# Performance work log

Measured on AMD Instinct MI355X. Metric: run time of the kernel, lower is better.

## Reference

```python
import jax, jax.numpy as jnp
import numpy as np

NL, B, L1, L2, D = 4, 64, 256, 256, 1024
LOGIT_SCALE = 1.0
BN_EPS = 1e-8


def setup_inputs() -> dict:
    key = jax.random.key(0)
    k1, k2, k3, k4, k5, k6 = jax.random.split(key, 6)
    reps1 = jax.random.normal(k1, (NL, B, L1, D), dtype=jnp.float32)
    reps2 = jax.random.normal(k2, (NL, B, L2, D), dtype=jnp.float32)
    len1 = jax.random.randint(k3, (B,), 1, L1 + 1)
    len2 = jax.random.randint(k4, (B,), 1, L2 + 1)
    w = jax.random.normal(k5, (1, NL), dtype=jnp.float32) * 0.1
    b = jax.random.normal(k6, (1,), dtype=jnp.float32) * 0.1
    return {"reps1": reps1, "reps2": reps2, "len1": len1, "len2": len2, "w": w, "b": b}


def reference(reps1, reps2, len1, len2, w, b):
    # reps: (NL, B, L, D) hidden states of selected layers, already (B-major per layer)
    neg = jnp.finfo(reps1.dtype).min
    # cosine-normalize along feature dim
    h1 = reps1 / jnp.linalg.norm(reps1, axis=-1, keepdims=True)
    h2 = reps2 / jnp.linalg.norm(reps2, axis=-1, keepdims=True)
    # similarity matrices for all layers at once: (NL, B, L1, L2)
    dots = jnp.einsum("lbid,lbjd->lbij", h1, h2)
    # ragged validity masks
    mask1 = jnp.arange(L1)[None, :] < len1[:, None]  # (B, L1)
    mask2 = jnp.arange(L2)[None, :] < len2[:, None]  # (B, L2)
    n1 = len1.astype(dots.dtype)
    n2 = len2.astype(dots.dtype)
    # max over valid rows i, mean over valid cols j  -> s1 (NL, B)
    max_i = jnp.max(jnp.where(mask1[None, :, :, None], dots, neg), axis=2)  # (NL,B,L2)
    s1 = jnp.sum(jnp.where(mask2[None], max_i, 0.0), axis=2) / n2[None]
    # max over valid cols j, mean over valid rows i  -> s2 (NL, B)
    max_j = jnp.max(jnp.where(mask2[None, :, None, :], dots, neg), axis=3)  # (NL,B,L1)
    s2 = jnp.sum(jnp.where(mask1[None], max_j, 0.0), axis=2) / n1[None]
    # harmonic mean (F1)
    feat = (2.0 * s1 * s2 / (s1 + s2)).T  # (B, NL)
    # BatchNorm1d(affine=False), training mode: batch stats, biased variance
    mean = jnp.mean(feat, axis=0, keepdims=True)
    var = jnp.mean((feat - mean) ** 2, axis=0, keepdims=True)
    feat = (feat - mean) / jnp.sqrt(var + BN_EPS)
    # final linear head + logit scale -> (B,)
    return LOGIT_SCALE * (feat @ w.T + b)[:, 0]
```

## Files before the change

kernel.cpp:

```cpp
#include <hip/hip_runtime.h>

#define NLAYERS 4
#define BATCH   64
#define LEN1    256
#define LEN2    256
#define DIM     1024
#define BKK     32
#define NKT     (DIM / BKK)
#define MHALF   128
#define PITCH   40

typedef _Float16 f16x8 __attribute__((ext_vector_type(8)));
typedef float    f32x4 __attribute__((ext_vector_type(4)));

__device__ __forceinline__ unsigned enc_f32(float v) {
  unsigned u = __float_as_uint(v);
  return (u & 0x80000000u) ? ~u : (u | 0x80000000u);
}
__device__ __forceinline__ float dec_f32(unsigned u) {
  return (u & 0x80000000u) ? __uint_as_float(u & 0x7fffffffu)
                           : __uint_as_float(~u);
}

__global__ __launch_bounds__(512, 4)
void bs_main(const float* __restrict__ reps1, const float* __restrict__ reps2,
             const int* __restrict__ len1, const int* __restrict__ len2,
             unsigned* __restrict__ colmax, float* __restrict__ s2acc) {
  __shared__ _Float16 Ah[2][MHALF * PITCH];
  __shared__ _Float16 Bh[2][LEN2 * PITCH];
  __shared__ float ssq1[MHALF];
  __shared__ float ssq2[LEN2];
  __shared__ float rowp[MHALF][4];
  __shared__ float colp[LEN2][2];
  __shared__ float redbuf[8];

  const int bid  = blockIdx.x;
  const int pair = ((bid >> 4) << 3) | (bid & 7);
  const int half = (bid >> 3) & 1;
  const int nl   = pair >> 6;
  const int bb   = pair & 63;
  const float* gA = reps1 + (size_t)pair * LEN1 * DIM + (size_t)half * MHALF * DIM;
  const float* gB = reps2 + (size_t)pair * LEN2 * DIM;

  const int tid  = threadIdx.x;
  const int lane = tid & 63;
  const int wid  = tid >> 6;
  const int wm   = wid >> 2;
  const int wn   = wid & 3;
  const int li   = lane & 15;
  const int lh   = lane >> 4;

  if (tid < MHALF) ssq1[tid] = 0.0f;
  if (tid >= 128 && tid < 384) ssq2[tid - 128] = 0.0f;

  f32x4 acc[4][4];
  #pragma unroll
  for (int a = 0; a < 4; ++a)
    #pragma unroll
    for (int c = 0; c < 4; ++c) acc[a][c] = 0.0f;

  float pssqA = 0.f, pssqB = 0.f;
  const int rA = tid >> 2;
  const int cA = (tid & 3) * 8;
  const int rB = tid >> 1;
  const int cB = (tid & 1) * 16;

  float4 ra[2], rb[4];

  auto issue_loads = [&](int kt) {
    const float4* a4 = (const float4*)(gA + (size_t)rA * DIM + kt * BKK + cA);
    ra[0] = a4[0];  ra[1] = a4[1];
    const float4* b4 = (const float4*)(gB + (size_t)rB * DIM + kt * BKK + cB);
    rb[0] = b4[0];  rb[1] = b4[1];  rb[2] = b4[2];  rb[3] = b4[3];
  };

  auto convert_write = [&](int buf) {
    {
      const float f0 = ra[0].x, f1 = ra[0].y, f2 = ra[0].z, f3 = ra[0].w;
      const float f4 = ra[1].x, f5 = ra[1].y, f6 = ra[1].z, f7 = ra[1].w;
      pssqA += f0*f0 + f1*f1 + f2*f2 + f3*f3 + f4*f4 + f5*f5 + f6*f6 + f7*f7;
      f16x8 hv;
      hv[0] = (_Float16)f0; hv[1] = (_Float16)f1; hv[2] = (_Float16)f2; hv[3] = (_Float16)f3;
      hv[4] = (_Float16)f4; hv[5] = (_Float16)f5; hv[6] = (_Float16)f6; hv[7] = (_Float16)f7;
      *(f16x8*)&Ah[buf][rA * PITCH + cA] = hv;
    }
    #pragma unroll
    for (int q = 0; q < 2; ++q) {
      const float f0 = rb[2*q].x,   f1 = rb[2*q].y,   f2 = rb[2*q].z,   f3 = rb[2*q].w;
      const float f4 = rb[2*q+1].x, f5 = rb[2*q+1].y, f6 = rb[2*q+1].z, f7 = rb[2*q+1].w;
      pssqB += f0*f0 + f1*f1 + f2*f2 + f3*f3 + f4*f4 + f5*f5 + f6*f6 + f7*f7;
      f16x8 hv;
      hv[0] = (_Float16)f0; hv[1] = (_Float16)f1; hv[2] = (_Float16)f2; hv[3] = (_Float16)f3;
      hv[4] = (_Float16)f4; hv[5] = (_Float16)f5; hv[6] = (_Float16)f6; hv[7] = (_Float16)f7;
      *(f16x8*)&Bh[buf][rB * PITCH + cB + 8*q] = hv;
    }
  };

  issue_loads(0);
  convert_write(0);
  __syncthreads();

  for (int kt = 0; kt < NKT; ++kt) {
    const int cur = kt & 1;
    const bool more = (kt + 1 < NKT);
    if (more) issue_loads(kt + 1);

    const _Float16* AhC = Ah[cur];
    const _Float16* BhC = Bh[cur];
    f16x8 af[4];
    #pragma unroll
    for (int fm = 0; fm < 4; ++fm) {
      const int r = wm * 64 + fm * 16 + li;
      af[fm] = *(const f16x8*)&AhC[r * PITCH + lh * 8];
    }
    #pragma unroll
    for (int fn = 0; fn < 4; ++fn) {
      const int r = wn * 64 + fn * 16 + li;
      const f16x8 bf = *(const f16x8*)&BhC[r * PITCH + lh * 8];
      #pragma unroll
      for (int fm = 0; fm < 4; ++fm)
        acc[fm][fn] = __builtin_amdgcn_mfma_f32_16x16x32_f16(af[fm], bf, acc[fm][fn], 0, 0, 0);
    }

    if (more) convert_write(cur ^ 1);
    __syncthreads();
  }

  atomicAdd(&ssq1[rA], pssqA);
  atomicAdd(&ssq2[rB], pssqB);
  __syncthreads();
  if (tid < MHALF) ssq1[tid] = 1.0f / sqrtf(ssq1[tid]);
  if (tid >= 128 && tid < 384) ssq2[tid - 128] = 1.0f / sqrtf(ssq2[tid - 128]);
  __syncthreads();

  const int n1 = len1[bb];
  const int n2 = len2[bb];

  float rn2v[4];
  bool  jv[4];
  #pragma unroll
  for (int fn = 0; fn < 4; ++fn) {
    const int j = wn * 64 + fn * 16 + li;
    rn2v[fn] = ssq2[j];
    jv[fn]   = (j < n2);
  }
  float rn1v[4][4];
  bool  iv[4][4];
  #pragma unroll
  for (int fm = 0; fm < 4; ++fm)
    #pragma unroll
    for (int rg = 0; rg < 4; ++rg) {
      const int i = wm * 64 + fm * 16 + lh * 4 + rg;
      rn1v[fm][rg] = ssq1[i];
      iv[fm][rg]   = (half * MHALF + i) < n1;
    }

  const float NEG = -3.402823466e38f;
  float rowm[4][4];
  float colm[4];
  #pragma unroll
  for (int fm = 0; fm < 4; ++fm)
    #pragma unroll
    for (int rg = 0; rg < 4; ++rg) rowm[fm][rg] = NEG;
  #pragma unroll
  for (int fn = 0; fn < 4; ++fn) colm[fn] = NEG;

  #pragma unroll
  for (int fm = 0; fm < 4; ++fm)
    #pragma unroll
    for (int fn = 0; fn < 4; ++fn)
      #pragma unroll
      for (int rg = 0; rg < 4; ++rg) {
        const float v = acc[fm][fn][rg] * rn1v[fm][rg] * rn2v[fn];
        if (jv[fn] && v > rowm[fm][rg]) rowm[fm][rg] = v;
        if (iv[fm][rg] && v > colm[fn]) colm[fn] = v;
      }

  #pragma unroll
  for (int m = 1; m <= 8; m <<= 1)
    #pragma unroll
    for (int fm = 0; fm < 4; ++fm)
      #pragma unroll
      for (int rg = 0; rg < 4; ++rg) {
        const float o = __shfl_xor(rowm[fm][rg], m, 64);
        rowm[fm][rg] = fmaxf(rowm[fm][rg], o);
      }
  #pragma unroll
  for (int m = 16; m <= 32; m <<= 1)
    #pragma unroll
    for (int fn = 0; fn < 4; ++fn) {
      const float o = __shfl_xor(colm[fn], m, 64);
      colm[fn] = fmaxf(colm[fn], o);
    }

  if (li == 0)
    #pragma unroll
    for (int fm = 0; fm < 4; ++fm)
      #pragma unroll
      for (int rg = 0; rg < 4; ++rg)
        rowp[wm * 64 + fm * 16 + lh * 4 + rg][wn] = rowm[fm][rg];
  if (lh == 0)
    #pragma unroll
    for (int fn = 0; fn < 4; ++fn)
      colp[wn * 64 + fn * 16 + li][wm] = colm[fn];
  __syncthreads();

  float c2 = 0.f;
  if (tid < MHALF) {
    const float rm = fmaxf(fmaxf(rowp[tid][0], rowp[tid][1]),
                           fmaxf(rowp[tid][2], rowp[tid][3]));
    if (half * MHALF + tid < n1) c2 = rm;
  }
  #pragma unroll
  for (int m = 1; m <= 32; m <<= 1) c2 += __shfl_xor(c2, m, 64);
  if (lane == 0) redbuf[wid] = c2;

  if (tid < LEN2) {
    const float cm = fmaxf(colp[tid][0], colp[tid][1]);
    atomicMax(&colmax[pair * LEN2 + tid], enc_f32(cm));
  }
  __syncthreads();
  if (tid == 0) {
    float s = 0.f;
    #pragma unroll
    for (int i = 0; i < 8; ++i) s += redbuf[i];
    atomicAdd(&s2acc[pair], s);
  }
}

__global__ void bs_combine(const unsigned* __restrict__ colmax,
                           const float* __restrict__ s2acc,
                           const int* __restrict__ len1, const int* __restrict__ len2,
                           float* __restrict__ feat) {
  __shared__ float part[4];
  const int p   = blockIdx.x;
  const int tid = threadIdx.x;
  const int bb  = p & 63;
  const int nl  = p >> 6;
  const int n1  = len1[bb];
  const int n2  = len2[bb];

  float c = 0.f;
  if (tid < n2) c = dec_f32(colmax[p * LEN2 + tid]);
  #pragma unroll
  for (int m = 1; m <= 32; m <<= 1) c += __shfl_xor(c, m, 64);
  if ((tid & 63) == 0) part[tid >> 6] = c;
  __syncthreads();
  if (tid == 0) {
    const float s1 = (part[0] + part[1] + part[2] + part[3]) / (float)n2;
    const float s2 = s2acc[p] / (float)n1;
    feat[bb * NLAYERS + nl] = 2.0f * s1 * s2 / (s1 + s2);
  }
}

__global__ void bs_head(const float* __restrict__ feat, const float* __restrict__ w,
                        const float* __restrict__ bias, float* __restrict__ out) {
  __shared__ float lds[NLAYERS][BATCH];
  const int tid = threadIdx.x;
  const int nl  = tid >> 6;
  const int b   = tid & 63;

  const float x = feat[b * NLAYERS + nl];
  float s = x;
  #pragma unroll
  for (int m = 1; m <= 32; m <<= 1) s += __shfl_xor(s, m, 64);
  const float mean = s / 64.0f;
  const float d = x - mean;
  float v = d * d;
  #pragma unroll
  for (int m = 1; m <= 32; m <<= 1) v += __shfl_xor(v, m, 64);
  const float var = v / 64.0f;
  const float y = d / sqrtf(var + 1e-8f);

  lds[nl][b] = y * w[nl];
  __syncthreads();
  if (tid < 64)
    out[tid] = lds[0][tid] + lds[1][tid] + lds[2][tid] + lds[3][tid] + bias[0];
}

extern "C" void kernel_launch(void* const* d_in, const int* in_sizes, int n_in,
                              void* d_out, int out_size, void* d_ws, size_t ws_size,
                              hipStream_t stream) {
  const float* reps1 = (const float*)d_in[0];
  const float* reps2 = (const float*)d_in[1];
  const int*   len1  = (const int*)d_in[2];
  const int*   len2  = (const int*)d_in[3];
  const float* w     = (const float*)d_in[4];
  const float* bias  = (const float*)d_in[5];

  unsigned* colmax = (unsigned*)d_ws;
  float*    s2acc  = (float*)((char*)d_ws + 256 * 256 * 4);
  float*    feat   = s2acc + 256;

  hipMemsetAsync(d_ws, 0, 256 * 256 * 4 + 2 * 256 * 4, stream);

  bs_main<<<2 * NLAYERS * BATCH, 512, 0, stream>>>(reps1, reps2, len1, len2,
                                                   colmax, s2acc);
  bs_combine<<<NLAYERS * BATCH, 256, 0, stream>>>(colmax, s2acc, len1, len2, feat);
  bs_head<<<1, 256, 0, stream>>>(feat, w, bias, (float*)d_out);
}
```

Baseline: 126.1 us.

## Process full 256x256 pair per 1024-thread block, dropping combine kernel and atomics

Each block now handles one whole (layer, batch) pair with 1024 threads (16 waves) instead of splitting rows across two 512-thread blocks. B is no longer loaded twice from global memory, so the global atomicMax on encoded column maxima, the workspace memset and the separate combine kernel all go away. Row and column reductions finish inside the block, which writes the F1 feature directly. The cost is a grid of 256 blocks on 256 CUs with larger LDS use per block, and fewer blocks to hide latency.

```diff
diff --git a/kernel.cpp b/kernel.cpp
--- a/kernel.cpp
+++ b/kernel.cpp
@@ -7,40 +7,28 @@
 #define DIM     1024
 #define BKK     32
 #define NKT     (DIM / BKK)
-#define MHALF   128
 #define PITCH   40
 
 typedef _Float16 f16x8 __attribute__((ext_vector_type(8)));
 typedef float    f32x4 __attribute__((ext_vector_type(4)));
 
-__device__ __forceinline__ unsigned enc_f32(float v) {
-  unsigned u = __float_as_uint(v);
-  return (u & 0x80000000u) ? ~u : (u | 0x80000000u);
-}
-__device__ __forceinline__ float dec_f32(unsigned u) {
-  return (u & 0x80000000u) ? __uint_as_float(u & 0x7fffffffu)
-                           : __uint_as_float(~u);
-}
-
-__global__ __launch_bounds__(512, 4)
+__global__ __launch_bounds__(1024, 4)
 void bs_main(const float* __restrict__ reps1, const float* __restrict__ reps2,
              const int* __restrict__ len1, const int* __restrict__ len2,
-             unsigned* __restrict__ colmax, float* __restrict__ s2acc) {
-  __shared__ _Float16 Ah[2][MHALF * PITCH];
+             float* __restrict__ feat) {
+  __shared__ _Float16 Ah[2][LEN1 * PITCH];
   __shared__ _Float16 Bh[2][LEN2 * PITCH];
-  __shared__ float ssq1[MHALF];
+  __shared__ float ssq1[LEN1];
   __shared__ float ssq2[LEN2];
-  __shared__ float rowp[MHALF][4];
-  __shared__ float colp[LEN2][2];
-  __shared__ float redbuf[8];
-
-  const int bid  = blockIdx.x;
-  const int pair = ((bid >> 4) << 3) | (bid & 7);
-  const int half = (bid >> 3) & 1;
-  const int nl   = pair >> 6;
-  const int bb   = pair & 63;
-  const float* gA = reps1 + (size_t)pair * LEN1 * DIM + (size_t)half * MHALF * DIM;
-  const float* gB = reps2 + (size_t)pair * LEN2 * DIM;
+  __shared__ float rowp[LEN1][4];
+  __shared__ float colp[LEN2][4];
+  __shared__ float redbuf[32];
+
+  const int bid = blockIdx.x;
+  const int nl  = bid >> 6;
+  const int bb  = bid & 63;
+  const float* gA = reps1 + (size_t)bid * LEN1 * DIM;
+  const float* gB = reps2 + (size_t)bid * LEN2 * DIM;
 
   const int tid  = threadIdx.x;
   const int lane = tid & 63;
@@ -50,8 +38,8 @@
   const int li   = lane & 15;
   const int lh   = lane >> 4;
 
-  if (tid < MHALF) ssq1[tid] = 0.0f;
-  if (tid >= 128 && tid < 384) ssq2[tid - 128] = 0.0f;
+  if (tid < 256)                  ssq1[tid] = 0.0f;
+  else if (tid < 512)             ssq2[tid - 256] = 0.0f;
 
   f32x4 acc[4][4];
   #pragma unroll
@@ -60,21 +48,20 @@
     for (int c = 0; c < 4; ++c) acc[a][c] = 0.0f;
 
   float pssqA = 0.f, pssqB = 0.f;
-  const int rA = tid >> 2;
-  const int cA = (tid & 3) * 8;
-  const int rB = tid >> 1;
-  const int cB = (tid & 1) * 16;
-
-  float4 ra[2], rb[4];
+  const int rS = tid >> 2;
+  const int cS = (tid & 3) * 8;
+
+  float4 ra[2], rb[2];
 
   auto issue_loads = [&](int kt) {
-    const float4* a4 = (const float4*)(gA + (size_t)rA * DIM + kt * BKK + cA);
+    const float4* a4 = (const float4*)(gA + (size_t)rS * DIM + kt * BKK + cS);
     ra[0] = a4[0];  ra[1] = a4[1];
-    const float4* b4 = (const float4*)(gB + (size_t)rB * DIM + kt * BKK + cB);
-    rb[0] = b4[0];  rb[1] = b4[1];  rb[2] = b4[2];  rb[3] = b4[3];
+    const float4* b4 = (const float4*)(gB + (size_t)rS * DIM + kt * BKK + cS);
+    rb[0] = b4[0];  rb[1] = b4[1];
   };
 
   auto convert_write = [&](int buf) {
+    const int idx = rS * PITCH + cS;
     {
       const float f0 = ra[0].x, f1 = ra[0].y, f2 = ra[0].z, f3 = ra[0].w;
       const float f4 = ra[1].x, f5 = ra[1].y, f6 = ra[1].z, f7 = ra[1].w;
@@ -82,17 +69,16 @@
       f16x8 hv;
       hv[0] = (_Float16)f0; hv[1] = (_Float16)f1; hv[2] = (_Float16)f2; hv[3] = (_Float16)f3;
       hv[4] = (_Float16)f4; hv[5] = (_Float16)f5; hv[6] = (_Float16)f6; hv[7] = (_Float16)f7;
-      *(f16x8*)&Ah[buf][rA * PITCH + cA] = hv;
-    }
-    #pragma unroll
-    for (int q = 0; q < 2; ++q) {
-      const float f0 = rb[2*q].x,   f1 = rb[2*q].y,   f2 = rb[2*q].z,   f3 = rb[2*q].w;
-      const float f4 = rb[2*q+1].x, f5 = rb[2*q+1].y, f6 = rb[2*q+1].z, f7 = rb[2*q+1].w;
+      *(f16x8*)&Ah[buf][idx] = hv;
+    }
+    {
+      const float f0 = rb[0].x, f1 = rb[0].y, f2 = rb[0].z, f3 = rb[0].w;
+      const float f4 = rb[1].x, f5 = rb[1].y, f6 = rb[1].z, f7 = rb[1].w;
       pssqB += f0*f0 + f1*f1 + f2*f2 + f3*f3 + f4*f4 + f5*f5 + f6*f6 + f7*f7;
       f16x8 hv;
       hv[0] = (_Float16)f0; hv[1] = (_Float16)f1; hv[2] = (_Float16)f2; hv[3] = (_Float16)f3;
       hv[4] = (_Float16)f4; hv[5] = (_Float16)f5; hv[6] = (_Float16)f6; hv[7] = (_Float16)f7;
-      *(f16x8*)&Bh[buf][rB * PITCH + cB + 8*q] = hv;
+      *(f16x8*)&Bh[buf][idx] = hv;
     }
   };
 
@@ -126,11 +112,11 @@
     __syncthreads();
   }
 
-  atomicAdd(&ssq1[rA], pssqA);
-  atomicAdd(&ssq2[rB], pssqB);
-  __syncthreads();
-  if (tid < MHALF) ssq1[tid] = 1.0f / sqrtf(ssq1[tid]);
-  if (tid >= 128 && tid < 384) ssq2[tid - 128] = 1.0f / sqrtf(ssq2[tid - 128]);
+  atomicAdd(&ssq1[rS], pssqA);
+  atomicAdd(&ssq2[rS], pssqB);
+  __syncthreads();
+  if (tid < 256)       ssq1[tid] = 1.0f / sqrtf(ssq1[tid]);
+  else if (tid < 512)  ssq2[tid - 256] = 1.0f / sqrtf(ssq2[tid - 256]);
   __syncthreads();
 
   const int n1 = len1[bb];
@@ -152,7 +138,7 @@
     for (int rg = 0; rg < 4; ++rg) {
       const int i = wm * 64 + fm * 16 + lh * 4 + rg;
       rn1v[fm][rg] = ssq1[i];
-      iv[fm][rg]   = (half * MHALF + i) < n1;
+      iv[fm][rg]   = (i < n1);
     }
 
   const float NEG = -3.402823466e38f;
@@ -205,50 +191,31 @@
       colp[wn * 64 + fn * 16 + li][wm] = colm[fn];
   __syncthreads();
 
-  float c2 = 0.f;
-  if (tid < MHALF) {
+  float c1 = 0.f, c2 = 0.f;
+  if (tid < 256) {
     const float rm = fmaxf(fmaxf(rowp[tid][0], rowp[tid][1]),
                            fmaxf(rowp[tid][2], rowp[tid][3]));
-    if (half * MHALF + tid < n1) c2 = rm;
-  }
-  #pragma unroll
-  for (int m = 1; m <= 32; m <<= 1) c2 += __shfl_xor(c2, m, 64);
-  if (lane == 0) redbuf[wid] = c2;
-
-  if (tid < LEN2) {
-    const float cm = fmaxf(colp[tid][0], colp[tid][1]);
-    atomicMax(&colmax[pair * LEN2 + tid], enc_f32(cm));
+    if (tid < n1) c2 = rm;
+    const float cm = fmaxf(fmaxf(colp[tid][0], colp[tid][1]),
+                           fmaxf(colp[tid][2], colp[tid][3]));
+    if (tid < n2) c1 = cm;
+  }
+  #pragma unroll
+  for (int m = 1; m <= 32; m <<= 1) {
+    c1 += __shfl_xor(c1, m, 64);
+    c2 += __shfl_xor(c2, m, 64);
+  }
+  if (lane == 0) {
+    redbuf[wid]      = c1;
+    redbuf[16 + wid] = c2;
   }
   __syncthreads();
   if (tid == 0) {
-    float s = 0.f;
-    #pragma unroll
-    for (int i = 0; i < 8; ++i) s += redbuf[i];
-    atomicAdd(&s2acc[pair], s);
-  }
-}
-
-__global__ void bs_combine(const unsigned* __restrict__ colmax,
-                           const float* __restrict__ s2acc,
-                           const int* __restrict__ len1, const int* __restrict__ len2,
-                           float* __restrict__ feat) {
-  __shared__ float part[4];
-  const int p   = blockIdx.x;
-  const int tid = threadIdx.x;
-  const int bb  = p & 63;
-  const int nl  = p >> 6;
-  const int n1  = len1[bb];
-  const int n2  = len2[bb];
-
-  float c = 0.f;
-  if (tid < n2) c = dec_f32(colmax[p * LEN2 + tid]);
-  #pragma unroll
-  for (int m = 1; m <= 32; m <<= 1) c += __shfl_xor(c, m, 64);
-  if ((tid & 63) == 0) part[tid >> 6] = c;
-  __syncthreads();
-  if (tid == 0) {
-    const float s1 = (part[0] + part[1] + part[2] + part[3]) / (float)n2;
-    const float s2 = s2acc[p] / (float)n1;
+    float s1s = 0.f, s2s = 0.f;
+    #pragma unroll
+    for (int i = 0; i < 16; ++i) { s1s += redbuf[i]; s2s += redbuf[16 + i]; }
+    const float s1 = s1s / (float)n2;
+    const float s2 = s2s / (float)n1;
     feat[bb * NLAYERS + nl] = 2.0f * s1 * s2 / (s1 + s2);
   }
 }
@@ -287,15 +254,8 @@
   const int*   len2  = (const int*)d_in[3];
   const float* w     = (const float*)d_in[4];
   const float* bias  = (const float*)d_in[5];
-
-  unsigned* colmax = (unsigned*)d_ws;
-  float*    s2acc  = (float*)((char*)d_ws + 256 * 256 * 4);
-  float*    feat   = s2acc + 256;
-
-  hipMemsetAsync(d_ws, 0, 256 * 256 * 4 + 2 * 256 * 4, stream);
-
-  bs_main<<<2 * NLAYERS * BATCH, 512, 0, stream>>>(reps1, reps2, len1, len2,
-                                                   colmax, s2acc);
-  bs_combine<<<NLAYERS * BATCH, 256, 0, stream>>>(colmax, s2acc, len1, len2, feat);
+  float* feat = (float*)d_ws;
+
+  bs_main<<<NLAYERS * BATCH, 1024, 0, stream>>>(reps1, reps2, len1, len2, feat);
   bs_head<<<1, 256, 0, stream>>>(feat, w, bias, (float*)d_out);
 }
```

New measurement: 113.1 us. 10.3% less time.
